# Optimization experiments

Hardware: AMD Instinct MI355X
Metric: run time of the kernel (lower is better)

The kernel has to match this reference:

```python
import jax, jax.numpy as jnp
import numpy as np

DIM = 128
NUM_HEADS = 4
WIN = 16  # effective window: window_size(8) * sqrt(dim_t=4)
N = WIN * WIN
B_ = 512
NW = 64


def _relative_position_index(wh, ww):
    coords = np.stack(np.meshgrid(np.arange(wh), np.arange(ww), indexing='ij'))  # (2,wh,ww)
    cf = coords.reshape(2, -1)
    rel = cf[:, :, None] - cf[:, None, :]  # (2,N,N)
    rel = rel.transpose(1, 2, 0).copy()
    rel[:, :, 0] += wh - 1
    rel[:, :, 1] += ww - 1
    rel[:, :, 0] *= 2 * ww - 1
    return rel.sum(-1).astype(np.int32)  # (N,N)


def setup_inputs() -> dict:
    key = jax.random.key(0)
    ks = jax.random.split(key, 7)
    inputs = jax.random.normal(ks[0], (B_, N, DIM), dtype=jnp.float32)
    mask = jax.random.normal(ks[1], (NW, N, N), dtype=jnp.float32)
    qkv_w = jax.random.normal(ks[2], (3 * DIM, DIM), dtype=jnp.float32) * 0.02
    qkv_b = jnp.zeros((3 * DIM,), dtype=jnp.float32)
    proj_w = jax.random.normal(ks[3], (DIM, DIM), dtype=jnp.float32) * 0.02
    proj_b = jnp.zeros((DIM,), dtype=jnp.float32)
    table_sz = (2 * WIN - 1) * (2 * WIN - 1)  # 961
    bias_table = jax.random.normal(ks[4], (table_sz, NUM_HEADS), dtype=jnp.float32) * 0.02
    rel_idx = jnp.asarray(_relative_position_index(WIN, WIN))  # (N,N) int32
    return {"inputs": inputs, "mask": mask, "qkv_w": qkv_w, "qkv_b": qkv_b,
            "proj_w": proj_w, "proj_b": proj_b, "bias_table": bias_table,
            "rel_idx": rel_idx}


def reference(inputs, mask, qkv_w, qkv_b, proj_w, proj_b, bias_table, rel_idx):
    B, Nn, C = inputs.shape
    H = bias_table.shape[1]
    Dh = C // H
    scale = Dh ** -0.5
    qkv = (inputs @ qkv_w.T + qkv_b).reshape(B, Nn, 3, H, Dh)
    qkv = jnp.transpose(qkv, (2, 0, 3, 1, 4))  # (3,B,H,N,Dh)
    q, k, v = qkv[0] * scale, qkv[1], qkv[2]
    attn = jnp.einsum('bhnd,bhmd->bhnm', q, k)  # (B,H,N,N)
    rpb = jnp.transpose(bias_table[rel_idx], (2, 0, 1))  # (H,N,N)
    attn = attn + rpb[None]
    nW = mask.shape[0]
    attn = attn.reshape(B // nW, nW, H, Nn, Nn) + mask[None, :, None]
    attn = jax.nn.softmax(attn.reshape(B, H, Nn, Nn), axis=-1)
    out = jnp.einsum('bhnm,bhmd->bhnd', attn, v)
    out = jnp.transpose(out, (0, 2, 1, 3)).reshape(B, Nn, C)
    return out @ proj_w.T + proj_b
```

## Files before the change

### kernel.cpp

```cpp
#include <hip/hip_runtime.h>

typedef __bf16 bf16;
typedef __bf16 bf16x8 __attribute__((ext_vector_type(8)));
typedef __bf16 bf16x4 __attribute__((ext_vector_type(4)));
typedef float f32x4 __attribute__((ext_vector_type(4)));

static __device__ __forceinline__ f32x4 mfma16(bf16x8 a, bf16x8 b, f32x4 c) {
  return __builtin_amdgcn_mfma_f32_16x16x32_bf16(a, b, c, 0, 0, 0);
}

static __device__ __forceinline__ bf16x8 ld_bf8(const float* __restrict__ p) {
  f32x4 a = *(const f32x4*)p;
  f32x4 b = *(const f32x4*)(p + 4);
  bf16x8 r;
  r[0] = (bf16)a[0]; r[1] = (bf16)a[1]; r[2] = (bf16)a[2]; r[3] = (bf16)a[3];
  r[4] = (bf16)b[0]; r[5] = (bf16)b[1]; r[6] = (bf16)b[2]; r[7] = (bf16)b[3];
  return r;
}

__global__ void k0_prep(const float* __restrict__ qw, const float* __restrict__ pw,
                        const float* __restrict__ bt, const int* __restrict__ ri,
                        const float* __restrict__ mask, bf16* __restrict__ wb,
                        bf16* __restrict__ pwb, bf16* __restrict__ rb,
                        bf16* __restrict__ mb) {
  const int bid = blockIdx.x;
  if (bid < 64) {
    const int t = bid * 256 + threadIdx.x;
    if (t < 12288) {
      f32x4 v = *(const f32x4*)(qw + (size_t)t * 4);
      bf16x4 o;
#pragma unroll
      for (int r = 0; r < 4; ++r) o[r] = (bf16)v[r];
      *(bf16x4*)(wb + (size_t)t * 4) = o;
    } else {
      const int u = t - 12288;
      f32x4 v = *(const f32x4*)(pw + (size_t)u * 4);
      bf16x4 o;
#pragma unroll
      for (int r = 0; r < 4; ++r) o[r] = (bf16)v[r];
      *(bf16x4*)(pwb + (size_t)u * 4) = o;
    }
  } else if (bid < 320) {
    const int t2 = (bid - 64) * 256 + threadIdx.x;
    const int idx = ri[t2];
    f32x4 v = *(const f32x4*)(bt + idx * 4);
#pragma unroll
    for (int h = 0; h < 4; ++h) rb[h * 65536 + t2] = (bf16)v[h];
  } else {
    const int mid = bid - 320;
#pragma unroll
    for (int it = 0; it < 4; ++it) {
      const size_t t = (size_t)mid * 1024 + it * 256 + threadIdx.x;
      f32x4 m4 = *(const f32x4*)(mask + t * 4);
      bf16x4 o;
#pragma unroll
      for (int r = 0; r < 4; ++r) o[r] = (bf16)m4[r];
      *(bf16x4*)(mb + t * 4) = o;
    }
  }
}

__global__ void __launch_bounds__(512, 2)
k_main(const float* __restrict__ x, const bf16* __restrict__ wb,
       const float* __restrict__ qb, const bf16* __restrict__ pwb,
       const float* __restrict__ pbias, const bf16* __restrict__ mb,
       const bf16* __restrict__ rb, float* __restrict__ out) {
  __shared__ bf16 xsm[256 * 128];
  __shared__ bf16 ksm[256 * 32];
  __shared__ bf16 vsm[32 * 256];
  __shared__ bf16 psm[8 * 1024];
  const int tid = threadIdx.x, wv = tid >> 6;
  const int ln = tid & 15, qd = (tid >> 4) & 3;
  const int bid = blockIdx.x;
  const int hb = (bid >> 3) & 1;
  const int b = ((bid >> 4) << 3) | (bid & 7);
  const int w = b & 63;
  bf16* pw_ = psm + wv * 1024;

  {
    const int cblk = tid & 15, r0 = tid >> 4;
#pragma unroll
    for (int j = 0; j < 8; ++j) {
      const int row = r0 + j * 32;
      bf16x8 v = ld_bf8(x + (size_t)(b * 256 + row) * 128 + cblk * 8);
      *(bf16x8*)(xsm + row * 128 + ((cblk ^ (row & 7)) * 8)) = v;
    }
  }

  const int n = hb * 128 + wv * 16 + ln;
  bf16x4 cmb[16];
#pragma unroll
  for (int mt = 0; mt < 16; ++mt)
    cmb[mt] = *(const bf16x4*)(mb + ((size_t)w * 256 + n) * 256 + mt * 16 + qd * 4);

  f32x4 acc_out[8];
#pragma unroll
  for (int ct2 = 0; ct2 < 8; ++ct2) acc_out[ct2] = (f32x4){0.f, 0.f, 0.f, 0.f};

  __syncthreads();

#pragma unroll 1
  for (int h = 0; h < 4; ++h) {
    bf16x8 qf;
    {
      bf16x8 xq[4];
#pragma unroll
      for (int ks = 0; ks < 4; ++ks)
        xq[ks] = *(const bf16x8*)(xsm + n * 128 + (((ks * 4 + qd) ^ (ln & 7)) * 8));
      f32x4 aq[2];
      aq[0] = (f32x4){0.f, 0.f, 0.f, 0.f};
      aq[1] = (f32x4){0.f, 0.f, 0.f, 0.f};
#pragma unroll
      for (int ct = 0; ct < 2; ++ct)
#pragma unroll
        for (int ks = 0; ks < 4; ++ks) {
          bf16x8 wf = *(const bf16x8*)(wb + (size_t)(h * 32 + ct * 16 + ln) * 128 +
                                       ks * 32 + qd * 8);
          aq[ct] = mfma16(wf, xq[ks], aq[ct]);
        }
#pragma unroll
      for (int ct = 0; ct < 2; ++ct) {
        const int c0 = ct * 16 + qd * 4;
        f32x4 b4 = *(const f32x4*)(qb + h * 32 + c0);
        bf16x4 o;
#pragma unroll
        for (int r = 0; r < 4; ++r)
          o[r] = (bf16)((aq[ct][r] + b4[r]) * 0.17677669529663689f);
        *(bf16x4*)(pw_ + ln * 32 + c0) = o;
      }
      qf = *(const bf16x8*)(pw_ + ln * 32 + qd * 8);
    }
    __syncthreads();

    {
      bf16x8 xf[2][4];
#pragma unroll
      for (int nt = 0; nt < 2; ++nt)
#pragma unroll
        for (int ks = 0; ks < 4; ++ks) {
          const int row = wv * 32 + nt * 16 + ln;
          xf[nt][ks] =
              *(const bf16x8*)(xsm + row * 128 + (((ks * 4 + qd) ^ (row & 7)) * 8));
        }
      f32x4 ak[2][2];
#pragma unroll
      for (int ct = 0; ct < 2; ++ct)
#pragma unroll
        for (int nt = 0; nt < 2; ++nt) ak[ct][nt] = (f32x4){0.f, 0.f, 0.f, 0.f};
#pragma unroll
      for (int ct = 0; ct < 2; ++ct)
#pragma unroll
        for (int ks = 0; ks < 4; ++ks) {
          bf16x8 wf = *(const bf16x8*)(wb + (size_t)(128 + h * 32 + ct * 16 + ln) * 128 +
                                       ks * 32 + qd * 8);
#pragma unroll
          for (int nt = 0; nt < 2; ++nt) ak[ct][nt] = mfma16(wf, xf[nt][ks], ak[ct][nt]);
        }
#pragma unroll
      for (int ct = 0; ct < 2; ++ct) {
        const int c0 = ct * 16 + qd * 4;
        f32x4 b4 = *(const f32x4*)(qb + 128 + h * 32 + c0);
        const int slot = ct * 2 + (qd >> 1), off = (qd & 1) * 4;
#pragma unroll
        for (int nt = 0; nt < 2; ++nt) {
          const int grow = wv * 32 + nt * 16 + ln;
          bf16x4 o;
#pragma unroll
          for (int r = 0; r < 4; ++r) o[r] = (bf16)(ak[ct][nt][r] + b4[r]);
          *(bf16x4*)(ksm + grow * 32 + ((slot ^ (grow & 3)) * 8) + off) = o;
        }
      }
      f32x4 av[2][2];
#pragma unroll
      for (int nt = 0; nt < 2; ++nt)
#pragma unroll
        for (int ct = 0; ct < 2; ++ct) av[nt][ct] = (f32x4){0.f, 0.f, 0.f, 0.f};
#pragma unroll
      for (int ks = 0; ks < 4; ++ks)
#pragma unroll
        for (int ct = 0; ct < 2; ++ct) {
          bf16x8 wf = *(const bf16x8*)(wb + (size_t)(256 + h * 32 + ct * 16 + ln) * 128 +
                                       ks * 32 + qd * 8);
#pragma unroll
          for (int nt = 0; nt < 2; ++nt) av[nt][ct] = mfma16(xf[nt][ks], wf, av[nt][ct]);
        }
#pragma unroll
      for (int nt = 0; nt < 2; ++nt)
#pragma unroll
        for (int ct = 0; ct < 2; ++ct) {
          const int c = ct * 16 + ln;
          const float bb = qb[256 + h * 32 + c];
          const int n0 = wv * 32 + nt * 16 + qd * 4;
          const int slot = n0 >> 3, off = (qd & 1) * 4;
          bf16x4 o;
#pragma unroll
          for (int r = 0; r < 4; ++r) o[r] = (bf16)(av[nt][ct][r] + bb);
          *(bf16x4*)(vsm + c * 256 + ((slot ^ (c & 7)) * 8) + off) = o;
        }
    }
    __syncthreads();

    {
      float sum = 0.f;
      f32x4 accO[2];
      accO[0] = (f32x4){0.f, 0.f, 0.f, 0.f};
      accO[1] = (f32x4){0.f, 0.f, 0.f, 0.f};
#pragma unroll
      for (int hq = 0; hq < 4; ++hq) {
        f32x4 acc[4];
#pragma unroll
        for (int mt = 0; mt < 4; ++mt) acc[mt] = (f32x4){0.f, 0.f, 0.f, 0.f};
#pragma unroll
        for (int mt = 0; mt < 4; ++mt) {
          const int m = hq * 64 + mt * 16 + ln;
          bf16x8 af = *(const bf16x8*)(ksm + m * 32 + ((qd ^ (m & 3)) * 8));
          acc[mt] = mfma16(af, qf, acc[mt]);
        }
#pragma unroll
        for (int mt = 0; mt < 4; ++mt) {
          const int mcol = hq * 64 + mt * 16 + qd * 4;
          bf16x4 r4 = *(const bf16x4*)(rb + (size_t)h * 65536 + n * 256 + mcol);
          const bf16x4 cm = cmb[hq * 4 + mt];
          bf16x4 pv;
#pragma unroll
          for (int r = 0; r < 4; ++r) {
            float p = __expf(acc[mt][r] + (float)cm[r] + (float)r4[r]);
            sum += p;
            pv[r] = (bf16)p;
          }
          *(bf16x4*)(pw_ + ln * 64 + (((mt * 2 + (qd >> 1)) ^ (ln & 7)) * 8) +
                     (qd & 1) * 4) = pv;
        }
#pragma unroll
        for (int ktl = 0; ktl < 2; ++ktl) {
          const int kt = hq * 2 + ktl;
          bf16x8 pf =
              *(const bf16x8*)(pw_ + ln * 64 + (((ktl * 4 + qd) ^ (ln & 7)) * 8));
#pragma unroll
          for (int ct = 0; ct < 2; ++ct) {
            const int d = ct * 16 + ln;
            bf16x8 vf =
                *(const bf16x8*)(vsm + d * 256 + (((kt * 4 + qd) ^ (d & 7)) * 8));
            accO[ct] = mfma16(pf, vf, accO[ct]);
          }
        }
      }
      sum += __shfl_xor(sum, 16);
      sum += __shfl_xor(sum, 32);
      const float linv = 1.0f / sum;
#pragma unroll
      for (int r = 0; r < 4; ++r) {
        const float lb = __shfl(linv, qd * 4 + r);
#pragma unroll
        for (int ct = 0; ct < 2; ++ct)
          pw_[(qd * 4 + r) * 40 + ct * 16 + ln] = (bf16)(accO[ct][r] * lb);
      }
      bf16x8 aof = *(const bf16x8*)(pw_ + ln * 40 + qd * 8);
#pragma unroll
      for (int ct2 = 0; ct2 < 8; ++ct2) {
        bf16x8 wpf =
            *(const bf16x8*)(pwb + (size_t)(ct2 * 16 + ln) * 128 + h * 32 + qd * 8);
        acc_out[ct2] = mfma16(aof, wpf, acc_out[ct2]);
      }
    }
  }

#pragma unroll
  for (int ct2 = 0; ct2 < 8; ++ct2) {
    const int col = ct2 * 16 + ln;
    const float bb = pbias[col];
#pragma unroll
    for (int r = 0; r < 4; ++r)
      out[(size_t)(b * 256 + hb * 128 + wv * 16 + qd * 4 + r) * 128 + col] =
          acc_out[ct2][r] + bb;
  }
}

extern "C" void kernel_launch(void* const* d_in, const int* in_sizes, int n_in,
                              void* d_out, int out_size, void* d_ws, size_t ws_size,
                              hipStream_t stream) {
  const float* x = (const float*)d_in[0];
  const float* mask = (const float*)d_in[1];
  const float* qkv_w = (const float*)d_in[2];
  const float* qkv_b = (const float*)d_in[3];
  const float* proj_w = (const float*)d_in[4];
  const float* proj_b = (const float*)d_in[5];
  const float* bias_table = (const float*)d_in[6];
  const int* rel_idx = (const int*)d_in[7];

  char* ws = (char*)d_ws;
  bf16* wb = (bf16*)ws;
  bf16* pwb = (bf16*)(ws + 98304);
  bf16* rb = (bf16*)(ws + 131072);
  bf16* mb = (bf16*)(ws + 655360);

  k0_prep<<<dim3(1344), dim3(256), 0, stream>>>(qkv_w, proj_w, bias_table, rel_idx,
                                                mask, wb, pwb, rb, mb);
  k_main<<<dim3(1024), dim3(512), 0, stream>>>(x, wb, qkv_b, pwb, proj_b, mb, rb,
                                               (float*)d_out);
}
```

Baseline: 365.1 us.

## Drop x shared staging, double-buffer K/V, read fp32 mask directly

```diff
diff --git a/kernel.cpp b/kernel.cpp
--- a/kernel.cpp
+++ b/kernel.cpp
@@ -20,9 +20,8 @@
 
 __global__ void k0_prep(const float* __restrict__ qw, const float* __restrict__ pw,
                         const float* __restrict__ bt, const int* __restrict__ ri,
-                        const float* __restrict__ mask, bf16* __restrict__ wb,
-                        bf16* __restrict__ pwb, bf16* __restrict__ rb,
-                        bf16* __restrict__ mb) {
+                        bf16* __restrict__ wb, bf16* __restrict__ pwb,
+                        bf16* __restrict__ rb) {
   const int bid = blockIdx.x;
   if (bid < 64) {
     const int t = bid * 256 + threadIdx.x;
@@ -40,34 +39,22 @@
       for (int r = 0; r < 4; ++r) o[r] = (bf16)v[r];
       *(bf16x4*)(pwb + (size_t)u * 4) = o;
     }
-  } else if (bid < 320) {
+  } else {
     const int t2 = (bid - 64) * 256 + threadIdx.x;
     const int idx = ri[t2];
     f32x4 v = *(const f32x4*)(bt + idx * 4);
 #pragma unroll
     for (int h = 0; h < 4; ++h) rb[h * 65536 + t2] = (bf16)v[h];
-  } else {
-    const int mid = bid - 320;
-#pragma unroll
-    for (int it = 0; it < 4; ++it) {
-      const size_t t = (size_t)mid * 1024 + it * 256 + threadIdx.x;
-      f32x4 m4 = *(const f32x4*)(mask + t * 4);
-      bf16x4 o;
-#pragma unroll
-      for (int r = 0; r < 4; ++r) o[r] = (bf16)m4[r];
-      *(bf16x4*)(mb + t * 4) = o;
-    }
   }
 }
 
-__global__ void __launch_bounds__(512, 2)
+__global__ void __launch_bounds__(512, 4)
 k_main(const float* __restrict__ x, const bf16* __restrict__ wb,
        const float* __restrict__ qb, const bf16* __restrict__ pwb,
-       const float* __restrict__ pbias, const bf16* __restrict__ mb,
+       const float* __restrict__ pbias, const float* __restrict__ mask,
        const bf16* __restrict__ rb, float* __restrict__ out) {
-  __shared__ bf16 xsm[256 * 128];
-  __shared__ bf16 ksm[256 * 32];
-  __shared__ bf16 vsm[32 * 256];
+  __shared__ bf16 ksm[2][256 * 32];
+  __shared__ bf16 vsm[2][32 * 256];
   __shared__ bf16 psm[8 * 1024];
   const int tid = threadIdx.x, wv = tid >> 6;
   const int ln = tid & 15, qd = (tid >> 4) & 3;
@@ -77,36 +64,27 @@
   const int w = b & 63;
   bf16* pw_ = psm + wv * 1024;
 
-  {
-    const int cblk = tid & 15, r0 = tid >> 4;
-#pragma unroll
-    for (int j = 0; j < 8; ++j) {
-      const int row = r0 + j * 32;
-      bf16x8 v = ld_bf8(x + (size_t)(b * 256 + row) * 128 + cblk * 8);
-      *(bf16x8*)(xsm + row * 128 + ((cblk ^ (row & 7)) * 8)) = v;
-    }
-  }
+  bf16x8 xf[2][4];
+#pragma unroll
+  for (int nt = 0; nt < 2; ++nt)
+#pragma unroll
+    for (int ks = 0; ks < 4; ++ks)
+      xf[nt][ks] = ld_bf8(x + (size_t)(b * 256 + ((hb ^ nt) << 7) + wv * 16 + ln) * 128 +
+                          ks * 32 + qd * 8);
 
   const int n = hb * 128 + wv * 16 + ln;
-  bf16x4 cmb[16];
-#pragma unroll
-  for (int mt = 0; mt < 16; ++mt)
-    cmb[mt] = *(const bf16x4*)(mb + ((size_t)w * 256 + n) * 256 + mt * 16 + qd * 4);
 
   f32x4 acc_out[8];
 #pragma unroll
   for (int ct2 = 0; ct2 < 8; ++ct2) acc_out[ct2] = (f32x4){0.f, 0.f, 0.f, 0.f};
-
-  __syncthreads();
 
 #pragma unroll 1
   for (int h = 0; h < 4; ++h) {
+    bf16* ks_ = &ksm[h & 1][0];
+    bf16* vs_ = &vsm[h & 1][0];
+
     bf16x8 qf;
     {
-      bf16x8 xq[4];
-#pragma unroll
-      for (int ks = 0; ks < 4; ++ks)
-        xq[ks] = *(const bf16x8*)(xsm + n * 128 + (((ks * 4 + qd) ^ (ln & 7)) * 8));
       f32x4 aq[2];
       aq[0] = (f32x4){0.f, 0.f, 0.f, 0.f};
       aq[1] = (f32x4){0.f, 0.f, 0.f, 0.f};
@@ -116,7 +94,7 @@
         for (int ks = 0; ks < 4; ++ks) {
           bf16x8 wf = *(const bf16x8*)(wb + (size_t)(h * 32 + ct * 16 + ln) * 128 +
                                        ks * 32 + qd * 8);
-          aq[ct] = mfma16(wf, xq[ks], aq[ct]);
+          aq[ct] = mfma16(wf, xf[0][ks], aq[ct]);
         }
 #pragma unroll
       for (int ct = 0; ct < 2; ++ct) {
@@ -130,18 +108,8 @@
       }
       qf = *(const bf16x8*)(pw_ + ln * 32 + qd * 8);
     }
-    __syncthreads();
 
     {
-      bf16x8 xf[2][4];
-#pragma unroll
-      for (int nt = 0; nt < 2; ++nt)
-#pragma unroll
-        for (int ks = 0; ks < 4; ++ks) {
-          const int row = wv * 32 + nt * 16 + ln;
-          xf[nt][ks] =
-              *(const bf16x8*)(xsm + row * 128 + (((ks * 4 + qd) ^ (row & 7)) * 8));
-        }
       f32x4 ak[2][2];
 #pragma unroll
       for (int ct = 0; ct < 2; ++ct)
@@ -163,11 +131,11 @@
         const int slot = ct * 2 + (qd >> 1), off = (qd & 1) * 4;
 #pragma unroll
         for (int nt = 0; nt < 2; ++nt) {
-          const int grow = wv * 32 + nt * 16 + ln;
+          const int grow = ((hb ^ nt) << 7) + wv * 16 + ln;
           bf16x4 o;
 #pragma unroll
           for (int r = 0; r < 4; ++r) o[r] = (bf16)(ak[ct][nt][r] + b4[r]);
-          *(bf16x4*)(ksm + grow * 32 + ((slot ^ (grow & 3)) * 8) + off) = o;
+          *(bf16x4*)(ks_ + grow * 32 + ((slot ^ (grow & 3)) * 8) + off) = o;
         }
       }
       f32x4 av[2][2];
@@ -190,12 +158,12 @@
         for (int ct = 0; ct < 2; ++ct) {
           const int c = ct * 16 + ln;
           const float bb = qb[256 + h * 32 + c];
-          const int n0 = wv * 32 + nt * 16 + qd * 4;
+          const int n0 = ((hb ^ nt) << 7) + wv * 16 + qd * 4;
           const int slot = n0 >> 3, off = (qd & 1) * 4;
           bf16x4 o;
 #pragma unroll
           for (int r = 0; r < 4; ++r) o[r] = (bf16)(av[nt][ct][r] + bb);
-          *(bf16x4*)(vsm + c * 256 + ((slot ^ (c & 7)) * 8) + off) = o;
+          *(bf16x4*)(vs_ + c * 256 + ((slot ^ (c & 7)) * 8) + off) = o;
         }
     }
     __syncthreads();
@@ -213,18 +181,18 @@
 #pragma unroll
         for (int mt = 0; mt < 4; ++mt) {
           const int m = hq * 64 + mt * 16 + ln;
-          bf16x8 af = *(const bf16x8*)(ksm + m * 32 + ((qd ^ (m & 3)) * 8));
+          bf16x8 af = *(const bf16x8*)(ks_ + m * 32 + ((qd ^ (m & 3)) * 8));
           acc[mt] = mfma16(af, qf, acc[mt]);
         }
 #pragma unroll
         for (int mt = 0; mt < 4; ++mt) {
           const int mcol = hq * 64 + mt * 16 + qd * 4;
+          f32x4 m4 = *(const f32x4*)(mask + ((size_t)w * 256 + n) * 256 + mcol);
           bf16x4 r4 = *(const bf16x4*)(rb + (size_t)h * 65536 + n * 256 + mcol);
-          const bf16x4 cm = cmb[hq * 4 + mt];
           bf16x4 pv;
 #pragma unroll
           for (int r = 0; r < 4; ++r) {
-            float p = __expf(acc[mt][r] + (float)cm[r] + (float)r4[r]);
+            float p = __expf(acc[mt][r] + m4[r] + (float)r4[r]);
             sum += p;
             pv[r] = (bf16)p;
           }
@@ -240,7 +208,7 @@
           for (int ct = 0; ct < 2; ++ct) {
             const int d = ct * 16 + ln;
             bf16x8 vf =
-                *(const bf16x8*)(vsm + d * 256 + (((kt * 4 + qd) ^ (d & 7)) * 8));
+                *(const bf16x8*)(vs_ + d * 256 + (((kt * 4 + qd) ^ (d & 7)) * 8));
             accO[ct] = mfma16(pf, vf, accO[ct]);
           }
         }
@@ -292,10 +260,9 @@
   bf16* wb = (bf16*)ws;
   bf16* pwb = (bf16*)(ws + 98304);
   bf16* rb = (bf16*)(ws + 131072);
-  bf16* mb = (bf16*)(ws + 655360);
-
-  k0_prep<<<dim3(1344), dim3(256), 0, stream>>>(qkv_w, proj_w, bias_table, rel_idx,
-                                                mask, wb, pwb, rb, mb);
-  k_main<<<dim3(1024), dim3(512), 0, stream>>>(x, wb, qkv_b, pwb, proj_b, mb, rb,
+
+  k0_prep<<<dim3(320), dim3(256), 0, stream>>>(qkv_w, proj_w, bias_table, rel_idx,
+                                               wb, pwb, rb);
+  k_main<<<dim3(1024), dim3(512), 0, stream>>>(x, wb, qkv_b, pwb, proj_b, mask, rb,
                                                (float*)d_out);
 }
```

Result: slower. 450.2 us (+23.3%).
